# Optimization experiments

Measured on AMD Instinct MI355X. Metric: run time of the kernel, lower is better.

The kernel has to match this reference:

```python
import jax, jax.numpy as jnp
import numpy as np

DIM = 768
HEADS = 12
HD = DIM // HEADS  # 64
WIN = 14
N = WIN * WIN  # 196
MLP_HID = 3072
EPS = 1e-6
SCALE = HD ** -0.5


def _ln(x, g, b):
    m = jnp.mean(x, axis=-1, keepdims=True)
    v = jnp.mean(jnp.square(x - m), axis=-1, keepdims=True)
    return (x - m) * jax.lax.rsqrt(v + EPS) * g + b


def _rel_table(rel):
    coords = jnp.arange(WIN)[:, None] - jnp.arange(WIN)[None, :] + (WIN - 1)
    return rel[coords]


def _window_partition(x, ws):
    B, H, W, C = x.shape
    pad_h = (ws - H % ws) % ws
    pad_w = (ws - W % ws) % ws
    x = jnp.pad(x, ((0, 0), (0, pad_h), (0, pad_w), (0, 0)))
    Hp, Wp = H + pad_h, W + pad_w
    x = x.reshape(B, Hp // ws, ws, Wp // ws, ws, C)
    win = x.transpose(0, 1, 3, 2, 4, 5).reshape(-1, ws, ws, C)
    return win, (Hp, Wp)


def _window_unpartition(win, ws, pad_hw, hw):
    Hp, Wp = pad_hw
    H, W = hw
    B = win.shape[0] // (Hp * Wp // ws // ws)
    x = win.reshape(B, Hp // ws, Wp // ws, ws, ws, -1)
    x = x.transpose(0, 1, 3, 2, 4, 5).reshape(B, Hp, Wp, -1)
    return x[:, :H, :W, :]


def _attention(x, qkv_w, qkv_b, proj_w, proj_b, rel_pos_h, rel_pos_w):
    Bw = x.shape[0]
    qkv = x.reshape(Bw, N, DIM) @ qkv_w + qkv_b  # (Bw, N, 3*DIM)
    qkv = qkv.reshape(Bw, N, 3, HEADS, HD).transpose(2, 0, 3, 1, 4)
    qkv = qkv.reshape(3, Bw * HEADS, N, HD)
    q, k, v = qkv[0], qkv[1], qkv[2]
    attn = jnp.einsum('bnd,bmd->bnm', q * SCALE, k)  # (Bw*H, N, N)
    Rh = _rel_table(rel_pos_h)
    Rw = _rel_table(rel_pos_w)
    r_q = q.reshape(-1, WIN, WIN, HD)
    rel_h = jnp.einsum('bhwc,hkc->bhwk', r_q, Rh)
    rel_w = jnp.einsum('bhwc,wkc->bhwk', r_q, Rw)
    attn = (attn.reshape(-1, WIN, WIN, WIN, WIN)
            + rel_h[:, :, :, :, None]
            + rel_w[:, :, :, None, :]).reshape(-1, N, N)
    attn = jax.nn.softmax(attn, axis=-1)
    out = jnp.einsum('bnm,bmd->bnd', attn, v)
    out = out.reshape(Bw, HEADS, WIN, WIN, HD).transpose(0, 2, 3, 1, 4)
    out = out.reshape(Bw, WIN, WIN, DIM)
    return out @ proj_w + proj_b


def setup_inputs() -> dict:
    key = jax.random.key(0)
    ks = jax.random.split(key, 10)
    s = 0.02
    return {
        'x': jax.random.normal(ks[0], (2, 64, 64, DIM), jnp.float32),
        'ln1_g': jnp.ones((DIM,), jnp.float32),
        'ln1_b': jnp.zeros((DIM,), jnp.float32),
        'qkv_w': jax.random.normal(ks[1], (DIM, 3 * DIM), jnp.float32) * s,
        'qkv_b': jax.random.normal(ks[2], (3 * DIM,), jnp.float32) * s,
        'proj_w': jax.random.normal(ks[3], (DIM, DIM), jnp.float32) * s,
        'proj_b': jax.random.normal(ks[4], (DIM,), jnp.float32) * s,
        'rel_pos_h': jax.random.normal(ks[5], (2 * WIN - 1, HD), jnp.float32) * s,
        'rel_pos_w': jax.random.normal(ks[6], (2 * WIN - 1, HD), jnp.float32) * s,
        'ln2_g': jnp.ones((DIM,), jnp.float32),
        'ln2_b': jnp.zeros((DIM,), jnp.float32),
        'fc1_w': jax.random.normal(ks[7], (DIM, MLP_HID), jnp.float32) * s,
        'fc1_b': jnp.zeros((MLP_HID,), jnp.float32),
        'fc2_w': jax.random.normal(ks[8], (MLP_HID, DIM), jnp.float32) * s,
        'fc2_b': jnp.zeros((DIM,), jnp.float32),
    }


def reference(x, ln1_g, ln1_b, qkv_w, qkv_b, proj_w, proj_b,
              rel_pos_h, rel_pos_w, ln2_g, ln2_b, fc1_w, fc1_b, fc2_w, fc2_b):
    B, H, W, _ = x.shape
    shortcut = x
    h = _ln(x, ln1_g, ln1_b)
    win, pad_hw = _window_partition(h, WIN)
    win = _attention(win, qkv_w, qkv_b, proj_w, proj_b, rel_pos_h, rel_pos_w)
    h = _window_unpartition(win, WIN, pad_hw, (H, W))
    x = shortcut + h  # drop_path prob 0 -> identity
    h = _ln(x, ln2_g, ln2_b)
    h = jax.nn.gelu(h @ fc1_w + fc1_b, approximate=False) @ fc2_w + fc2_b
    return x + h
```

## Files before the change

### kernel.cpp

```cpp
#include <hip/hip_runtime.h>
#include <hip/hip_bf16.h>
#include <math.h>


#define DIMC 768
#define HEADS 12
#define WIN 14
#define NTOK 196
#define NWIN 50
#define MROWS 9800
#define YROWS 8192
#define MLP_HID 3072

using bf16x8 = __attribute__((ext_vector_type(8))) short;
using f32x4  = __attribute__((ext_vector_type(4))) float;

__device__ __forceinline__ float bf2f(unsigned short u) {
    return __uint_as_float(((unsigned)u) << 16);
}
__device__ __forceinline__ unsigned short f2bf(float f) {
    unsigned u = __float_as_uint(f);
    unsigned r = (u + 0x7fffu + ((u >> 16) & 1u)) >> 16;
    return (unsigned short)r;
}
__device__ __forceinline__ void gl2lds16(const unsigned short* g, unsigned short* l) {
    __builtin_amdgcn_global_load_lds(
        (const __attribute__((address_space(1))) void*)g,
        (__attribute__((address_space(3))) void*)l, 16, 0, 0);
}

__device__ __forceinline__ float fast_gelu(float v) {
    float u = v * 0.70710678118654752f;
    float a = fabsf(u);
    float t = __builtin_amdgcn_rcpf(fmaf(0.3275911f, a, 1.0f));
    float p = t * fmaf(t, fmaf(t, fmaf(t, fmaf(t, 1.061405429f, -1.453152027f),
                       1.421413741f), -0.284496736f), 0.254829592f);
    float e = __expf(-u * u);
    float er = fmaf(-p, e, 1.0f);
    er = copysignf(er, v);
    return 0.5f * v * (1.0f + er);
}

__global__ __launch_bounds__(256) void transpose_all(
        const float* __restrict__ Wq, unsigned short* __restrict__ Tq,
        const float* __restrict__ Wp, unsigned short* __restrict__ Tp,
        const float* __restrict__ W1, unsigned short* __restrict__ T1,
        const float* __restrict__ W2, unsigned short* __restrict__ T2) {
    int id = blockIdx.x;
    const float* W; unsigned short* Wt; int K, N, nbx, rel;
    if (id < 432)       { W = Wq; Wt = Tq; K = 768;  N = 2304; nbx = 36; rel = id; }
    else if (id < 576)  { W = Wp; Wt = Tp; K = 768;  N = 768;  nbx = 12; rel = id - 432; }
    else if (id < 1152) { W = W1; Wt = T1; K = 768;  N = 3072; nbx = 48; rel = id - 576; }
    else                { W = W2; Wt = T2; K = 3072; N = 768;  nbx = 12; rel = id - 1152; }
    int bx = rel % nbx, by = rel / nbx;
    __shared__ float t[64][65];
    int k0 = by << 6, n0 = bx << 6;
    int tn = threadIdx.x & 63;
    int tk = threadIdx.x >> 6;
    #pragma unroll
    for (int r = 0; r < 16; r++) {
        int k = tk + r * 4;
        t[k][tn] = W[(size_t)(k0 + k) * N + n0 + tn];
    }
    __syncthreads();
    #pragma unroll
    for (int r = 0; r < 16; r++) {
        int n = tk + r * 4;
        Wt[(size_t)(n0 + n) * K + k0 + tn] = f2bf(t[tn][n]);
    }
}

__global__ __launch_bounds__(256) void ln1_win_kernel(
        const float* __restrict__ x, const float* __restrict__ g,
        const float* __restrict__ b, unsigned short* __restrict__ h1) {
    int tid = threadIdx.x;
    int row = blockIdx.x * 4 + (tid >> 6);
    int lane = tid & 63;
    if (row >= MROWS) return;
    int w = row / NTOK, t = row % NTOK;
    int bi = w / 25, wr = w % 25;
    int gy = (wr / 5) * WIN + t / WIN;
    int gx = (wr % 5) * WIN + t % WIN;
    unsigned short* out = h1 + (size_t)row * DIMC;
    if (gy >= 64 || gx >= 64) {
        #pragma unroll
        for (int j = 0; j < 12; j++) out[lane + 64 * j] = 0;
        return;
    }
    const float* xr = x + ((size_t)((bi * 64 + gy) * 64 + gx)) * DIMC;
    float v[12], s = 0.f;
    #pragma unroll
    for (int j = 0; j < 12; j++) { v[j] = xr[lane + 64 * j]; s += v[j]; }
    #pragma unroll
    for (int o = 32; o > 0; o >>= 1) s += __shfl_xor(s, o);
    float mean = s * (1.f / 768.f);
    float q = 0.f;
    #pragma unroll
    for (int j = 0; j < 12; j++) { float d = v[j] - mean; q += d * d; }
    #pragma unroll
    for (int o = 32; o > 0; o >>= 1) q += __shfl_xor(q, o);
    float inv = rsqrtf(q * (1.f / 768.f) + 1e-6f);
    #pragma unroll
    for (int j = 0; j < 12; j++) {
        int c = lane + 64 * j;
        out[c] = f2bf((v[j] - mean) * inv * g[c] + b[c]);
    }
}

__global__ __launch_bounds__(256) void ln2_kernel(
        const float* __restrict__ y, const float* __restrict__ g,
        const float* __restrict__ b, unsigned short* __restrict__ h2) {
    int tid = threadIdx.x;
    int row = blockIdx.x * 4 + (tid >> 6);
    int lane = tid & 63;
    const float* xr = y + (size_t)row * DIMC;
    float v[12], s = 0.f;
    #pragma unroll
    for (int j = 0; j < 12; j++) { v[j] = xr[lane + 64 * j]; s += v[j]; }
    #pragma unroll
    for (int o = 32; o > 0; o >>= 1) s += __shfl_xor(s, o);
    float mean = s * (1.f / 768.f);
    float q = 0.f;
    #pragma unroll
    for (int j = 0; j < 12; j++) { float d = v[j] - mean; q += d * d; }
    #pragma unroll
    for (int o = 32; o > 0; o >>= 1) q += __shfl_xor(q, o);
    float inv = rsqrtf(q * (1.f / 768.f) + 1e-6f);
    unsigned short* out = h2 + (size_t)row * DIMC;
    #pragma unroll
    for (int j = 0; j < 12; j++) {
        int c = lane + 64 * j;
        out[c] = f2bf((v[j] - mean) * inv * g[c] + b[c]);
    }
}

__global__ __launch_bounds__(256) void build_aug(
        const unsigned short* __restrict__ qkvb,
        const float* __restrict__ relph, const float* __restrict__ relpw,
        unsigned short* __restrict__ Aaug, unsigned short* __restrict__ Vt) {
    __shared__ unsigned short qs[208 * 72];
    __shared__ unsigned short rt[64 * 72];
    int tid = threadIdx.x;
    int bh = blockIdx.x, w = bh / HEADS, head = bh % HEADS;
    int lane = tid & 63, wave = tid >> 6;
    int l15 = lane & 15, q4 = lane >> 4, q8 = q4 * 8;
    size_t base = (size_t)w * NTOK * 2304 + head * 64;
    unsigned short* ab = Aaug + (size_t)bh * 256 * 96;

    for (int e = tid; e < 196 * 8; e += 256) {
        int t = e >> 3, s8 = (e & 7) * 8;
        bf16x8 qv = *(const bf16x8*)&qkvb[base + (size_t)t * 2304 + s8];
        *(bf16x8*)&qs[t * 72 + s8] = qv;
        bf16x8 qo;
        #pragma unroll
        for (int jj = 0; jj < 8; jj++)
            qo[jj] = (short)f2bf(bf2f((unsigned short)qv[jj]) * 0.125f);
        *(bf16x8*)&ab[t * 96 + s8] = qo;
    }
    for (int e = tid; e < 12 * 8; e += 256) {
        bf16x8 z = {};
        *(bf16x8*)&qs[(196 + (e >> 3)) * 72 + (e & 7) * 8] = z;
    }
    for (int e = tid; e < 64 * 8; e += 256) {
        int r = e >> 3, s8 = (e & 7) * 8;
        bf16x8 ov = {};
        if (r < 54) {
            const float* src = (r < 27 ? relph + (size_t)r * 64
                                       : relpw + (size_t)(r - 27) * 64) + s8;
            #pragma unroll
            for (int jj = 0; jj < 8; jj++) ov[jj] = (short)f2bf(src[jj]);
        }
        *(bf16x8*)&rt[r * 72 + s8] = ov;
    }
    for (int e = tid; e < 60 * 12; e += 256) {
        bf16x8 z = {};
        *(bf16x8*)&ab[(size_t)(196 + e / 12) * 96 + (e % 12) * 8] = z;
    }
    for (int e = tid; e < 196; e += 256) {
        ab[e * 96 + 92] = 0; ab[e * 96 + 93] = 0;
        ab[e * 96 + 94] = 0; ab[e * 96 + 95] = 0;
    }
    __syncthreads();

    #pragma unroll
    for (int t = 0; t < 4; t++) {
        int it = wave * 4 + t;
        if (it >= 13) break;
        bf16x8 a0 = *(bf16x8*)&qs[(it * 16 + l15) * 72 + q8];
        bf16x8 a1 = *(bf16x8*)&qs[(it * 16 + l15) * 72 + 32 + q8];
        #pragma unroll
        for (int rt4 = 0; rt4 < 4; rt4++) {
            bf16x8 b0 = *(bf16x8*)&rt[(rt4 * 16 + l15) * 72 + q8];
            bf16x8 b1 = *(bf16x8*)&rt[(rt4 * 16 + l15) * 72 + 32 + q8];
            f32x4 d4 = {};
            d4 = __builtin_amdgcn_mfma_f32_16x16x32_bf16(a0, b0, d4, 0, 0, 0);
            d4 = __builtin_amdgcn_mfma_f32_16x16x32_bf16(a1, b1, d4, 0, 0, 0);
            int rcol = rt4 * 16 + l15;
            #pragma unroll
            for (int r = 0; r < 4; r++) {
                int i = it * 16 + q4 * 4 + r;
                if (i < 196 && rcol < 54) {
                    if (rcol < 27) {
                        int c = 13 + i / 14 - rcol;
                        if (c >= 0 && c < 14) ab[i * 96 + 64 + c] = f2bf(d4[r]);
                    } else {
                        int c = 13 + i % 14 - (rcol - 27);
                        if (c >= 0 && c < 14) ab[i * 96 + 78 + c] = f2bf(d4[r]);
                    }
                }
            }
        }
    }

    unsigned short* vtb = Vt + (size_t)bh * 64 * 224;
    for (int e = tid; e < 196 * 8; e += 256) {
        int j = e >> 3, dg = (e & 7) * 8;
        bf16x8 vv = *(const bf16x8*)&qkvb[base + 1536 + (size_t)j * 2304 + dg];
        #pragma unroll
        for (int k = 0; k < 8; k++)
            vtb[(size_t)(dg + k) * 224 + j] = (unsigned short)vv[k];
    }
    for (int e = tid; e < 64 * 28; e += 256)
        vtb[(size_t)(e / 28) * 224 + 196 + (e % 28)] = 0;
}

__global__ __launch_bounds__(256) void attn_mfma(
        const unsigned short* __restrict__ qkvb,
        const unsigned short* __restrict__ Aaug,
        const unsigned short* __restrict__ Vt,
        unsigned short* __restrict__ out) {
    __shared__ unsigned short Kk[208 * 64];
    __shared__ unsigned short Koh[208 * 40];
    __shared__ unsigned short Pls[4][64 * 44];
    int tid = threadIdx.x;
    int bh = blockIdx.x, w = bh / HEADS, head = bh % HEADS;
    int wave = tid >> 6, lane = tid & 63;
    int l15 = lane & 15, q4 = lane >> 4, q8 = q4 * 8;
    size_t kbase = (size_t)w * NTOK * 2304 + head * 64 + 768;
    {
        int sw = ((lane & 7) ^ (lane >> 3)) * 8;
        for (int r0 = wave * 8; r0 < 208; r0 += 32) {
            int grow = r0 + (lane >> 3);
            if (grow > 195) grow = 195;
            gl2lds16(&qkvb[kbase + (size_t)grow * 2304 + sw],
                     &Kk[r0 * 64 + lane * 8]);
        }
    }
    bf16x8 z8 = {};
    for (int e = tid; e < 208 * 5; e += 256)
        *(bf16x8*)&Koh[(e / 5) * 40 + (e % 5) * 8] = z8;
    __syncthreads();
    for (int e = tid; e < 196; e += 256) {
        Koh[e * 40 + e / WIN] = 0x3F80;
        Koh[e * 40 + 14 + e % WIN] = 0x3F80;
    }
    bf16x8 af[4][3];
    const unsigned short* abse = Aaug + (size_t)bh * 256 * 96;
    #pragma unroll
    for (int it = 0; it < 4; it++)
        #pragma unroll
        for (int c = 0; c < 3; c++)
            af[it][c] = *(const bf16x8*)&abse[(size_t)(wave * 64 + it * 16 + l15) * 96 + c * 32 + q8];
    __syncthreads();

    const unsigned short* vtb = Vt + (size_t)bh * 64 * 224;
    f32x4 o[4][4] = {};
    float lacc[4][4] = {{0.f}};
    bf16x8 bv[4];
    #pragma unroll
    for (int dt = 0; dt < 4; dt++)
        bv[dt] = *(const bf16x8*)&vtb[(dt * 16 + l15) * 224 + q8];

    for (int jp = 0; jp < 7; jp++) {
        f32x4 s[4][2] = {};
        #pragma unroll
        for (int half = 0; half < 2; half++) {
            int jt = jp * 2 + half;
            if (jt < 13) {
                int krow = jt * 16 + l15;
                #pragma unroll
                for (int c = 0; c < 2; c++) {
                    bf16x8 bk = *(bf16x8*)&Kk[krow * 64 + (((c * 4 + q4) ^ (l15 & 7)) * 8)];
                    #pragma unroll
                    for (int it = 0; it < 4; it++)
                        s[it][half] = __builtin_amdgcn_mfma_f32_16x16x32_bf16(
                            af[it][c], bk, s[it][half], 0, 0, 0);
                }
                bf16x8 bo = *(bf16x8*)&Koh[krow * 40 + q8];
                #pragma unroll
                for (int it = 0; it < 4; it++)
                    s[it][half] = __builtin_amdgcn_mfma_f32_16x16x32_bf16(
                        af[it][2], bo, s[it][half], 0, 0, 0);
            }
        }
        #pragma unroll
        for (int half = 0; half < 2; half++) {
            int jt = jp * 2 + half;
            bool valid = (jt < 13) && (jt * 16 + l15) < 196;
            #pragma unroll
            for (int it = 0; it < 4; it++)
                #pragma unroll
                for (int r = 0; r < 4; r++) {
                    float p = valid ? __expf(s[it][half][r]) : 0.f;
                    unsigned short pb = f2bf(p);
                    lacc[it][r] += bf2f(pb);
                    Pls[wave][(it * 16 + q4 * 4 + r) * 44 + half * 16 + l15] = pb;
                }
        }
        asm volatile("s_waitcnt lgkmcnt(0)" ::: "memory");
        bf16x8 ap[4];
        #pragma unroll
        for (int it = 0; it < 4; it++)
            ap[it] = *(bf16x8*)&Pls[wave][(it * 16 + l15) * 44 + q8];
        bf16x8 bvn[4];
        if (jp < 6) {
            #pragma unroll
            for (int dt = 0; dt < 4; dt++)
                bvn[dt] = *(const bf16x8*)&vtb[(dt * 16 + l15) * 224 + (jp + 1) * 32 + q8];
        }
        #pragma unroll
        for (int dt = 0; dt < 4; dt++)
            #pragma unroll
            for (int it = 0; it < 4; it++)
                o[it][dt] = __builtin_amdgcn_mfma_f32_16x16x32_bf16(
                    ap[it], bv[dt], o[it][dt], 0, 0, 0);
        if (jp < 6) {
            #pragma unroll
            for (int dt = 0; dt < 4; dt++) bv[dt] = bvn[dt];
        }
    }
    #pragma unroll
    for (int it = 0; it < 4; it++)
        #pragma unroll
        for (int r = 0; r < 4; r++) {
            float v = lacc[it][r];
            v += __shfl_xor(v, 1); v += __shfl_xor(v, 2);
            v += __shfl_xor(v, 4); v += __shfl_xor(v, 8);
            lacc[it][r] = 1.f / v;
        }
    #pragma unroll
    for (int it = 0; it < 4; it++) {
        int i0 = wave * 64 + it * 16 + q4 * 4;
        #pragma unroll
        for (int r = 0; r < 4; r++) {
            if (i0 + r < 196) {
                size_t rowb = (size_t)(w * NTOK + i0 + r) * DIMC + head * 64;
                #pragma unroll
                for (int dt = 0; dt < 4; dt++)
                    out[rowb + dt * 16 + l15] = f2bf(o[it][dt][r] * lacc[it][r]);
            }
        }
    }
}

template <int EPI, int BN>
__global__ __launch_bounds__(256) void mgemm(
        const unsigned short* __restrict__ A, const unsigned short* __restrict__ Bt,
        const float* __restrict__ bias, void* __restrict__ Cout,
        const float* __restrict__ resid, int M, int Nn, int K,
        int nbx, int nby) {
    const int NI = BN / 32;
    constexpr int LPT = (BN == 128) ? 4 : 3;
    __shared__ unsigned short As[3][128 * 32];
    __shared__ unsigned short Bs[3][BN * 32];
    int tid = threadIdx.x;
    int lane = tid & 63, wave = tid >> 6;
    int l15 = lane & 15, q4 = lane >> 4;
    int xq8 = (q4 ^ ((l15 >> 1) & 3)) * 8;
    int id = blockIdx.x;
    int per = nbx * 8;
    int s = id / per;
    int rem = id - s * per;
    int rmax = nby - s * 8; if (rmax > 8) rmax = 8;
    int bx = rem / rmax;
    int r_ = rem - bx * rmax;
    int by = s * 8 + r_;
    int m0 = by << 7, n0 = bx * BN;
    int wm = (wave >> 1) * 64, wn = (wave & 1) * (BN / 2);
    int srow0 = wave * 32 + (lane >> 2);
    int srow1 = srow0 + 16;
    int sseg = ((lane & 3) ^ ((lane >> 3) & 3)) * 8;
    int rmA0 = m0 + srow0; if (rmA0 >= M) rmA0 = M - 1;
    int rmA1 = m0 + srow1; if (rmA1 >= M) rmA1 = M - 1;
    const unsigned short* gA0 = A + (size_t)rmA0 * K + sseg;
    const unsigned short* gA1 = A + (size_t)rmA1 * K + sseg;
    int browB = (BN == 128) ? srow0 : (wave * 16 + (lane >> 2));
    const unsigned short* gB0 = Bt + (size_t)(n0 + browB) * K + sseg;
    const unsigned short* gB1 = Bt + (size_t)(n0 + srow1) * K + sseg;
    int lofsA = wave * 1024 + lane * 8;
    int lofsB = ((BN == 128) ? wave * 1024 : wave * 512) + lane * 8;
    f32x4 acc[4][NI] = {};
    int nt = K >> 5;
    gl2lds16(gA0, &As[0][lofsA]);
    gl2lds16(gA1, &As[0][lofsA + 512]);
    gl2lds16(gB0, &Bs[0][lofsB]);
    if (BN == 128) gl2lds16(gB1, &Bs[0][lofsB + 512]);
    if (nt > 1) {
        gl2lds16(gA0 + 32, &As[1][lofsA]);
        gl2lds16(gA1 + 32, &As[1][lofsA + 512]);
        gl2lds16(gB0 + 32, &Bs[1][lofsB]);
        if (BN == 128) gl2lds16(gB1 + 32, &Bs[1][lofsB + 512]);
    }
    int cur = 0;
    for (int t = 0; t < nt; ++t) {
        if (t + 1 < nt) {
            asm volatile("s_waitcnt vmcnt(%0)" :: "i"(LPT) : "memory");
        } else {
            asm volatile("s_waitcnt vmcnt(0)" ::: "memory");
        }
        __builtin_amdgcn_s_barrier();
        if (t + 2 < nt) {
            int b2 = cur + 2; if (b2 >= 3) b2 -= 3;
            int kn = (t + 2) << 5;
            gl2lds16(gA0 + kn, &As[b2][lofsA]);
            gl2lds16(gA1 + kn, &As[b2][lofsA + 512]);
            gl2lds16(gB0 + kn, &Bs[b2][lofsB]);
            if (BN == 128) gl2lds16(gB1 + kn, &Bs[b2][lofsB + 512]);
        }
        bf16x8 bfr[NI];
        #pragma unroll
        for (int ni = 0; ni < NI; ni++)
            bfr[ni] = *(bf16x8*)&Bs[cur][(wn + ni * 16 + l15) * 32 + xq8];
        #pragma unroll
        for (int mi = 0; mi < 4; mi++) {
            bf16x8 afr = *(bf16x8*)&As[cur][(wm + mi * 16 + l15) * 32 + xq8];
            #pragma unroll
            for (int ni = 0; ni < NI; ni++)
                acc[mi][ni] = __builtin_amdgcn_mfma_f32_16x16x32_bf16(
                    afr, bfr[ni], acc[mi][ni], 0, 0, 0);
        }
        cur = (cur == 2) ? 0 : cur + 1;
    }
    int q4r = (lane >> 4) * 4;
    #pragma unroll
    for (int mi = 0; mi < 4; mi++) {
        #pragma unroll
        for (int r = 0; r < 4; r++) {
            int row = m0 + wm + mi * 16 + q4r + r;
            if (row >= M) continue;
            if (EPI == 2) {
                int w = row / NTOK, t = row % NTOK;
                int bi = w / 25, wr = w % 25;
                int gy = (wr / 5) * WIN + t / WIN;
                int gx = (wr % 5) * WIN + t % WIN;
                if (gy >= 64 || gx >= 64) continue;
                size_t orow = ((size_t)((bi * 64 + gy) * 64 + gx)) * DIMC;
                #pragma unroll
                for (int ni = 0; ni < NI; ni++) {
                    int col = n0 + wn + ni * 16 + l15;
                    float v = acc[mi][ni][r] + bias[col];
                    ((float*)Cout)[orow + col] = resid[orow + col] + v;
                }
            } else {
                #pragma unroll
                for (int ni = 0; ni < NI; ni++) {
                    int col = n0 + wn + ni * 16 + l15;
                    float v = acc[mi][ni][r] + bias[col];
                    if (EPI == 0) {
                        ((unsigned short*)Cout)[(size_t)row * Nn + col] = f2bf(v);
                    } else if (EPI == 1) {
                        v = fast_gelu(v);
                        ((unsigned short*)Cout)[(size_t)row * Nn + col] = f2bf(v);
                    } else {
                        ((float*)Cout)[(size_t)row * Nn + col] =
                            resid[(size_t)row * Nn + col] + v;
                    }
                }
            }
        }
    }
}

extern "C" void kernel_launch(void* const* d_in, const int* in_sizes, int n_in,
                              void* d_out, int out_size, void* d_ws, size_t ws_size,
                              hipStream_t stream) {
    const float* x      = (const float*)d_in[0];
    const float* ln1_g  = (const float*)d_in[1];
    const float* ln1_b  = (const float*)d_in[2];
    const float* qkv_w  = (const float*)d_in[3];
    const float* qkv_b  = (const float*)d_in[4];
    const float* proj_w = (const float*)d_in[5];
    const float* proj_b = (const float*)d_in[6];
    const float* rel_h  = (const float*)d_in[7];
    const float* rel_w  = (const float*)d_in[8];
    const float* ln2_g  = (const float*)d_in[9];
    const float* ln2_b  = (const float*)d_in[10];
    const float* fc1_w  = (const float*)d_in[11];
    const float* fc1_b  = (const float*)d_in[12];
    const float* fc2_w  = (const float*)d_in[13];
    const float* fc2_b  = (const float*)d_in[14];
    float* out = (float*)d_out;
    char* ws = (char*)d_ws;

    unsigned short* wt_qkv  = (unsigned short*)(ws);
    unsigned short* wt_proj = (unsigned short*)(ws + 3538944);
    unsigned short* wt_fc1  = (unsigned short*)(ws + 4718592);
    unsigned short* wt_fc2  = (unsigned short*)(ws + 9437184);
    unsigned short* qkvb    = (unsigned short*)(ws + 14155776);
    float*          yb      = (float*)        (ws + 14155776);
    unsigned short* h2      = (unsigned short*)(ws + 39321600);
    unsigned short* h1      = (unsigned short*)(ws + 59314176);
    unsigned short* attn_o  = h1;
    unsigned short* zb      = h1;
    unsigned short* Aaug    = (unsigned short*)(ws + 74366976);
    unsigned short* Vt      = (unsigned short*)(ws + 103858176);

    transpose_all<<<1728, 256, 0, stream>>>(
        qkv_w, wt_qkv, proj_w, wt_proj, fc1_w, wt_fc1, fc2_w, wt_fc2);

    ln1_win_kernel<<<(MROWS + 3) / 4, 256, 0, stream>>>(x, ln1_g, ln1_b, h1);

    mgemm<0, 128><<<18 * 77, 256, 0, stream>>>(
        h1, wt_qkv, qkv_b, qkvb, nullptr, MROWS, 2304, DIMC, 18, 77);

    build_aug<<<NWIN * HEADS, 256, 0, stream>>>(qkvb, rel_h, rel_w, Aaug, Vt);

    attn_mfma<<<NWIN * HEADS, 256, 0, stream>>>(qkvb, Aaug, Vt, attn_o);

    mgemm<2, 64><<<12 * 77, 256, 0, stream>>>(
        attn_o, wt_proj, proj_b, yb, x, MROWS, DIMC, DIMC, 12, 77);

    ln2_kernel<<<YROWS / 4, 256, 0, stream>>>(yb, ln2_g, ln2_b, h2);

    mgemm<1, 128><<<24 * 64, 256, 0, stream>>>(
        h2, wt_fc1, fc1_b, zb, nullptr, YROWS, MLP_HID, DIMC, 24, 64);

    mgemm<3, 64><<<12 * 64, 256, 0, stream>>>(
        zb, wt_fc2, fc2_b, out, yb, YROWS, DIMC, MLP_HID, 12, 64);
}
```

Measured before the change: 415.3 us.

## Fuse relative-position augmentation build into attention kernel via shared memory

Merges build_aug and attn_mfma into one kernel. Q, V-transpose and the relative-position bias columns now live in a reused LDS buffer instead of round-tripping through the global Aaug/Vt workspaces. K is read directly from global memory inside the score loop rather than staged in LDS. This removes one launch and the global write and reread of the augmented Q and V. In exchange, LDS use per block grows to about 81KB, which limits occupancy, and the K loads sit uncached in the inner loop.

```diff
diff --git a/kernel.cpp b/kernel.cpp
--- a/kernel.cpp
+++ b/kernel.cpp
@@ -134,32 +134,34 @@
     }
 }
 
-__global__ __launch_bounds__(256) void build_aug(
+__global__ __launch_bounds__(256) void attn_fused(
         const unsigned short* __restrict__ qkvb,
         const float* __restrict__ relph, const float* __restrict__ relpw,
-        unsigned short* __restrict__ Aaug, unsigned short* __restrict__ Vt) {
-    __shared__ unsigned short qs[208 * 72];
-    __shared__ unsigned short rt[64 * 72];
+        unsigned short* __restrict__ out) {
+    __shared__ __align__(16) char smem[81152];
+    unsigned short* qs   = (unsigned short*)smem;
+    unsigned short* rt   = (unsigned short*)(smem + 29952);
+    unsigned short* Koh  = (unsigned short*)smem;
+    unsigned short* Pls  = (unsigned short*)(smem + 15680);
+    unsigned short* Vt   = (unsigned short*)(smem + 39168);
+    unsigned short* relc = (unsigned short*)(smem + 67840);
     int tid = threadIdx.x;
     int bh = blockIdx.x, w = bh / HEADS, head = bh % HEADS;
-    int lane = tid & 63, wave = tid >> 6;
+    int wave = tid >> 6, lane = tid & 63;
     int l15 = lane & 15, q4 = lane >> 4, q8 = q4 * 8;
-    size_t base = (size_t)w * NTOK * 2304 + head * 64;
-    unsigned short* ab = Aaug + (size_t)bh * 256 * 96;
+    size_t qb = (size_t)w * NTOK * 2304 + head * 64;
+    size_t kb = qb + 768, vb = qb + 1536;
 
     for (int e = tid; e < 196 * 8; e += 256) {
         int t = e >> 3, s8 = (e & 7) * 8;
-        bf16x8 qv = *(const bf16x8*)&qkvb[base + (size_t)t * 2304 + s8];
-        *(bf16x8*)&qs[t * 72 + s8] = qv;
-        bf16x8 qo;
-        #pragma unroll
-        for (int jj = 0; jj < 8; jj++)
-            qo[jj] = (short)f2bf(bf2f((unsigned short)qv[jj]) * 0.125f);
-        *(bf16x8*)&ab[t * 96 + s8] = qo;
-    }
-    for (int e = tid; e < 12 * 8; e += 256) {
+        *(bf16x8*)&qs[t * 72 + s8] = *(const bf16x8*)&qkvb[qb + (size_t)t * 2304 + s8];
+    }
+    {
         bf16x8 z = {};
-        *(bf16x8*)&qs[(196 + (e >> 3)) * 72 + (e & 7) * 8] = z;
+        for (int e = tid; e < 12 * 8; e += 256)
+            *(bf16x8*)&qs[(196 + (e >> 3)) * 72 + (e & 7) * 8] = z;
+        for (int e = tid; e < 208 * 4; e += 256)
+            *(bf16x8*)&relc[(e >> 2) * 32 + (e & 3) * 8] = z;
     }
     for (int e = tid; e < 64 * 8; e += 256) {
         int r = e >> 3, s8 = (e & 7) * 8;
@@ -172,16 +174,30 @@
         }
         *(bf16x8*)&rt[r * 72 + s8] = ov;
     }
-    for (int e = tid; e < 60 * 12; e += 256) {
-        bf16x8 z = {};
-        *(bf16x8*)&ab[(size_t)(196 + e / 12) * 96 + (e % 12) * 8] = z;
-    }
-    for (int e = tid; e < 196; e += 256) {
-        ab[e * 96 + 92] = 0; ab[e * 96 + 93] = 0;
-        ab[e * 96 + 94] = 0; ab[e * 96 + 95] = 0;
-    }
+    for (int e = tid; e < 196 * 8; e += 256) {
+        int j = e >> 3, dg = (e & 7) * 8;
+        bf16x8 vv = *(const bf16x8*)&qkvb[vb + (size_t)j * 2304 + dg];
+        #pragma unroll
+        for (int k = 0; k < 8; k++)
+            Vt[(dg + k) * 224 + j] = (unsigned short)vv[k];
+    }
+    for (int e = tid; e < 64 * 28; e += 256)
+        Vt[(e / 28) * 224 + 196 + (e % 28)] = 0;
     __syncthreads();
 
+    bf16x8 af[4][3];
+    #pragma unroll
+    for (int it = 0; it < 4; it++) {
+        int arow = wave * 64 + it * 16 + l15;
+        if (arow > 195) arow = 195;
+        #pragma unroll
+        for (int c = 0; c < 2; c++) {
+            bf16x8 t8 = *(bf16x8*)&qs[arow * 72 + c * 32 + q8];
+            #pragma unroll
+            for (int jj = 0; jj < 8; jj++)
+                af[it][c][jj] = (short)f2bf(bf2f((unsigned short)t8[jj]) * 0.125f);
+        }
+    }
     #pragma unroll
     for (int t = 0; t < 4; t++) {
         int it = wave * 4 + t;
@@ -200,76 +216,46 @@
             for (int r = 0; r < 4; r++) {
                 int i = it * 16 + q4 * 4 + r;
                 if (i < 196 && rcol < 54) {
+                    int cc = -1;
                     if (rcol < 27) {
                         int c = 13 + i / 14 - rcol;
-                        if (c >= 0 && c < 14) ab[i * 96 + 64 + c] = f2bf(d4[r]);
+                        if (c >= 0 && c < 14) cc = c;
                     } else {
                         int c = 13 + i % 14 - (rcol - 27);
-                        if (c >= 0 && c < 14) ab[i * 96 + 78 + c] = f2bf(d4[r]);
+                        if (c >= 0 && c < 14) cc = 14 + c;
                     }
+                    if (cc >= 0)
+                        relc[i * 32 + (((cc >> 3) ^ (i & 3)) << 3) + (cc & 7)] =
+                            f2bf(d4[r]);
                 }
             }
         }
     }
-
-    unsigned short* vtb = Vt + (size_t)bh * 64 * 224;
-    for (int e = tid; e < 196 * 8; e += 256) {
-        int j = e >> 3, dg = (e & 7) * 8;
-        bf16x8 vv = *(const bf16x8*)&qkvb[base + 1536 + (size_t)j * 2304 + dg];
-        #pragma unroll
-        for (int k = 0; k < 8; k++)
-            vtb[(size_t)(dg + k) * 224 + j] = (unsigned short)vv[k];
-    }
-    for (int e = tid; e < 64 * 28; e += 256)
-        vtb[(size_t)(e / 28) * 224 + 196 + (e % 28)] = 0;
-}
-
-__global__ __launch_bounds__(256) void attn_mfma(
-        const unsigned short* __restrict__ qkvb,
-        const unsigned short* __restrict__ Aaug,
-        const unsigned short* __restrict__ Vt,
-        unsigned short* __restrict__ out) {
-    __shared__ unsigned short Kk[208 * 64];
-    __shared__ unsigned short Koh[208 * 40];
-    __shared__ unsigned short Pls[4][64 * 44];
-    int tid = threadIdx.x;
-    int bh = blockIdx.x, w = bh / HEADS, head = bh % HEADS;
-    int wave = tid >> 6, lane = tid & 63;
-    int l15 = lane & 15, q4 = lane >> 4, q8 = q4 * 8;
-    size_t kbase = (size_t)w * NTOK * 2304 + head * 64 + 768;
+    __syncthreads();
     {
-        int sw = ((lane & 7) ^ (lane >> 3)) * 8;
-        for (int r0 = wave * 8; r0 < 208; r0 += 32) {
-            int grow = r0 + (lane >> 3);
-            if (grow > 195) grow = 195;
-            gl2lds16(&qkvb[kbase + (size_t)grow * 2304 + sw],
-                     &Kk[r0 * 64 + lane * 8]);
-        }
-    }
-    bf16x8 z8 = {};
-    for (int e = tid; e < 208 * 5; e += 256)
-        *(bf16x8*)&Koh[(e / 5) * 40 + (e % 5) * 8] = z8;
+        bf16x8 z = {};
+        for (int e = tid; e < 196 * 5; e += 256)
+            *(bf16x8*)&Koh[(e / 5) * 40 + (e % 5) * 8] = z;
+    }
     __syncthreads();
     for (int e = tid; e < 196; e += 256) {
         Koh[e * 40 + e / WIN] = 0x3F80;
         Koh[e * 40 + 14 + e % WIN] = 0x3F80;
     }
-    bf16x8 af[4][3];
-    const unsigned short* abse = Aaug + (size_t)bh * 256 * 96;
-    #pragma unroll
-    for (int it = 0; it < 4; it++)
-        #pragma unroll
-        for (int c = 0; c < 3; c++)
-            af[it][c] = *(const bf16x8*)&abse[(size_t)(wave * 64 + it * 16 + l15) * 96 + c * 32 + q8];
+    #pragma unroll
+    for (int it = 0; it < 4; it++) {
+        int arow = wave * 64 + it * 16 + l15;
+        if (arow > 195) arow = 195;
+        af[it][2] = *(bf16x8*)&relc[arow * 32 + ((q4 ^ (arow & 3)) << 3)];
+    }
     __syncthreads();
 
-    const unsigned short* vtb = Vt + (size_t)bh * 64 * 224;
     f32x4 o[4][4] = {};
     float lacc[4][4] = {{0.f}};
     bf16x8 bv[4];
     #pragma unroll
     for (int dt = 0; dt < 4; dt++)
-        bv[dt] = *(const bf16x8*)&vtb[(dt * 16 + l15) * 224 + q8];
+        bv[dt] = *(bf16x8*)&Vt[(dt * 16 + l15) * 224 + q8];
 
     for (int jp = 0; jp < 7; jp++) {
         f32x4 s[4][2] = {};
@@ -278,21 +264,23 @@
             int jt = jp * 2 + half;
             if (jt < 13) {
                 int krow = jt * 16 + l15;
+                if (krow > 195) krow = 195;
+                const unsigned short* kr = qkvb + kb + (size_t)krow * 2304;
+                bf16x8 bk0 = *(const bf16x8*)&kr[q8];
+                bf16x8 bk1 = *(const bf16x8*)&kr[32 + q8];
+                bf16x8 bo  = *(bf16x8*)&Koh[krow * 40 + q8];
                 #pragma unroll
-                for (int c = 0; c < 2; c++) {
-                    bf16x8 bk = *(bf16x8*)&Kk[krow * 64 + (((c * 4 + q4) ^ (l15 & 7)) * 8)];
-                    #pragma unroll
-                    for (int it = 0; it < 4; it++)
-                        s[it][half] = __builtin_amdgcn_mfma_f32_16x16x32_bf16(
-                            af[it][c], bk, s[it][half], 0, 0, 0);
-                }
-                bf16x8 bo = *(bf16x8*)&Koh[krow * 40 + q8];
-                #pragma unroll
-                for (int it = 0; it < 4; it++)
+                for (int it = 0; it < 4; it++) {
+                    s[it][half] = __builtin_amdgcn_mfma_f32_16x16x32_bf16(
+                        af[it][0], bk0, s[it][half], 0, 0, 0);
+                    s[it][half] = __builtin_amdgcn_mfma_f32_16x16x32_bf16(
+                        af[it][1], bk1, s[it][half], 0, 0, 0);
                     s[it][half] = __builtin_amdgcn_mfma_f32_16x16x32_bf16(
                         af[it][2], bo, s[it][half], 0, 0, 0);
+                }
             }
         }
+        unsigned short* pw = Pls + wave * (64 * 44);
         #pragma unroll
         for (int half = 0; half < 2; half++) {
             int jt = jp * 2 + half;
@@ -304,19 +292,19 @@
                     float p = valid ? __expf(s[it][half][r]) : 0.f;
                     unsigned short pb = f2bf(p);
                     lacc[it][r] += bf2f(pb);
-                    Pls[wave][(it * 16 + q4 * 4 + r) * 44 + half * 16 + l15] = pb;
+                    pw[(it * 16 + q4 * 4 + r) * 44 + half * 16 + l15] = pb;
                 }
         }
         asm volatile("s_waitcnt lgkmcnt(0)" ::: "memory");
         bf16x8 ap[4];
         #pragma unroll
         for (int it = 0; it < 4; it++)
-            ap[it] = *(bf16x8*)&Pls[wave][(it * 16 + l15) * 44 + q8];
+            ap[it] = *(bf16x8*)&pw[(it * 16 + l15) * 44 + q8];
         bf16x8 bvn[4];
         if (jp < 6) {
             #pragma unroll
             for (int dt = 0; dt < 4; dt++)
-                bvn[dt] = *(const bf16x8*)&vtb[(dt * 16 + l15) * 224 + (jp + 1) * 32 + q8];
+                bvn[dt] = *(bf16x8*)&Vt[(dt * 16 + l15) * 224 + (jp + 1) * 32 + q8];
         }
         #pragma unroll
         for (int dt = 0; dt < 4; dt++)
@@ -502,8 +490,6 @@
     unsigned short* h1      = (unsigned short*)(ws + 59314176);
     unsigned short* attn_o  = h1;
     unsigned short* zb      = h1;
-    unsigned short* Aaug    = (unsigned short*)(ws + 74366976);
-    unsigned short* Vt      = (unsigned short*)(ws + 103858176);
 
     transpose_all<<<1728, 256, 0, stream>>>(
         qkv_w, wt_qkv, proj_w, wt_proj, fc1_w, wt_fc1, fc2_w, wt_fc2);
@@ -513,9 +499,7 @@
     mgemm<0, 128><<<18 * 77, 256, 0, stream>>>(
         h1, wt_qkv, qkv_b, qkvb, nullptr, MROWS, 2304, DIMC, 18, 77);
 
-    build_aug<<<NWIN * HEADS, 256, 0, stream>>>(qkvb, rel_h, rel_w, Aaug, Vt);
-
-    attn_mfma<<<NWIN * HEADS, 256, 0, stream>>>(qkvb, Aaug, Vt, attn_o);
+    attn_fused<<<NWIN * HEADS, 256, 0, stream>>>(qkvb, rel_h, rel_w, attn_o);
 
     mgemm<2, 64><<<12 * 77, 256, 0, stream>>>(
         attn_o, wt_proj, proj_b, yb, x, MROWS, DIMC, DIMC, 12, 77);
```

Result: faster. 406.8 us (-2.0%).
